# Performance work log

Measured on AMD Instinct MI355X. Metric: run time of the kernel, lower is better.

Reference implementation:

```python
import jax, jax.numpy as jnp
import numpy as np

N_NODES = 131072
IN_F = 512
HID = 512
H = 8
DH = HID // H
B = 1024  # batch_size (num graphs); static for jit
LN_EPS = 1e-5


def setup_inputs() -> dict:
    key = jax.random.key(0)
    ks = jax.random.split(key, 12)
    # equal-size segments (128 nodes/graph), sorted as in PyG batching
    batch = (jnp.arange(N_NODES) // (N_NODES // B)).astype(jnp.int32)
    s = 0.02
    return {
        "x": jax.random.normal(ks[0], (N_NODES, IN_F), jnp.float32),
        "batch": batch,
        "query": jax.random.normal(ks[1], (H, DH), jnp.float32) * s,
        "key_w": jax.random.normal(ks[2], (HID, IN_F), jnp.float32) * s,
        "key_b": jnp.zeros((HID,), jnp.float32),
        "value_w": jax.random.normal(ks[3], (HID, IN_F), jnp.float32) * s,
        "value_b": jnp.zeros((HID,), jnp.float32),
        "out_w": jax.random.normal(ks[4], (IN_F, HID), jnp.float32) * s,
        "out_b": jnp.zeros((IN_F,), jnp.float32),
        "gate_w": jax.random.normal(ks[5], (IN_F, 2 * IN_F), jnp.float32) * s,
        "gate_b": jnp.zeros((IN_F,), jnp.float32),
        "ln_w": jnp.ones((IN_F,), jnp.float32),
        "ln_b": jnp.zeros((IN_F,), jnp.float32),
    }


def reference(x, batch, query, key_w, key_b, value_w, value_b, out_w, out_b,
              gate_w, gate_b, ln_w, ln_b):
    N = x.shape[0]
    # projections (dense GEMMs)
    keys = (x @ key_w.T + key_b).reshape(N, H, DH)
    values = (x @ value_w.T + value_b).reshape(N, H, DH)
    # per-node attention logits against shared per-head query: [N, H]
    scores = jnp.einsum('nhd,hd->nh', keys, query)
    # segment softmax over nodes within each graph
    smax = jax.ops.segment_max(scores, batch, num_segments=B)  # [B, H]
    smax = jnp.where(jnp.isfinite(smax), smax, 0.0)            # guard empty graphs
    e = jnp.exp(scores - smax[batch])
    ssum = jax.ops.segment_sum(e, batch, num_segments=B)       # [B, H]
    w = e / jnp.maximum(ssum[batch], 1e-12)                    # [N, H]  (dropout is eval-mode identity)
    # attention-weighted pooling of values: [B, H, DH] -> [B, HID]
    pooled = jax.ops.segment_sum(w[:, :, None] * values, batch, num_segments=B)
    ctx = pooled.reshape(B, HID) @ out_w.T + out_b             # [B, IN_F]
    # gating with per-graph mean pool
    counts = jax.ops.segment_sum(jnp.ones((N,), x.dtype), batch, num_segments=B)
    avg = jax.ops.segment_sum(x, batch, num_segments=B) / jnp.maximum(counts, 1.0)[:, None]
    gate = jax.nn.sigmoid(jnp.concatenate([ctx, avg], axis=1) @ gate_w.T + gate_b)
    ctx = gate * ctx + (1.0 - gate) * avg
    emb = jnp.where(counts[:, None] > 0, ctx, 0.0)             # empty graphs stay zero
    # LayerNorm
    mu = emb.mean(-1, keepdims=True)
    var = emb.var(-1, keepdims=True)
    return (emb - mu) / jnp.sqrt(var + LN_EPS) * ln_w + ln_b
```

## Files before the change

### kernel.cpp

```cpp
#include <hip/hip_runtime.h>
#include <hip/hip_bf16.h>

typedef short short8 __attribute__((ext_vector_type(8)));
typedef float f32x4 __attribute__((ext_vector_type(4)));

#define NGRAPH 1024
#define NPG    128
#define INF    512
#define NHEAD  8
#define CH     32

__device__ __forceinline__ ushort f2b(float f){
  __hip_bfloat16 h(f);
  union { __hip_bfloat16 h; ushort u; } v; v.h = h; return v.u;
}
__device__ __forceinline__ float b2f_lo(unsigned u){
  union { unsigned u; float f; } v; v.u = u << 16; return v.f;
}
__device__ __forceinline__ float b2f_hi(unsigned u){
  union { unsigned u; float f; } v; v.u = u & 0xffff0000u; return v.f;
}

__global__ void k_prep(const float* __restrict__ q, const float* __restrict__ kw,
                       float* __restrict__ kq,
                       const float* __restrict__ vw, ushort* __restrict__ vwb,
                       const float* __restrict__ ow, ushort* __restrict__ owb,
                       const float* __restrict__ gw, ushort* __restrict__ gwb){
  const int b = blockIdx.x, t = threadIdx.x;
  if(b < 16){
    int h = b >> 1, f = (b & 1)*256 + t;
    float s = 0.f;
    #pragma unroll 8
    for(int d = 0; d < 64; d++)
      s += q[h*64 + d] * kw[(size_t)(h*64 + d)*INF + f];
    kq[h*INF + f] = s;
  } else if(b < 16 + 1024){
    int i = (b - 16)*256 + t;   vwb[i] = f2b(vw[i]);
  } else if(b < 16 + 2048){
    int i = (b - 1040)*256 + t; owb[i] = f2b(ow[i]);
  } else {
    int i = (b - 2064)*256 + t; gwb[i] = f2b(gw[i]);
  }
}

__global__ __launch_bounds__(128, 2) void k_graph(
    const float* __restrict__ x, const float* __restrict__ kq,
    ushort* __restrict__ xw_b, float* __restrict__ avg_f, ushort* __restrict__ avg_b){
  __shared__ __align__(16) ushort xs[CH*INF];
  __shared__ __align__(16) float  sc[CH*NHEAD];
  __shared__ float mEf[3*NHEAD];

  const int t = threadIdx.x, lane = t & 63, w = t >> 6;
  const int col = lane & 15, kg = lane >> 4;
  const int g = blockIdx.x;
  const int node = w*16 + col;

  short8 bfrag[16];
  {
    const bool ok = (col < 8);
    const float* kqr = kq + col*INF;
    #pragma unroll
    for(int ks = 0; ks < 16; ks++){
      short8 v = short8{0,0,0,0,0,0,0,0};
      if(ok){
        float4 p0 = *(const float4*)(kqr + ks*32 + kg*8);
        float4 p1 = *(const float4*)(kqr + ks*32 + kg*8 + 4);
        v[0]=(short)f2b(p0.x); v[1]=(short)f2b(p0.y); v[2]=(short)f2b(p0.z); v[3]=(short)f2b(p0.w);
        v[4]=(short)f2b(p1.x); v[5]=(short)f2b(p1.y); v[6]=(short)f2b(p1.z); v[7]=(short)f2b(p1.w);
      }
      bfrag[ks] = v;
    }
  }

  if(t < NHEAD){ mEf[t] = -1e30f; mEf[NHEAD + t] = 0.f; }

  float acc[NHEAD][4];
  #pragma unroll
  for(int h = 0; h < NHEAD; h++)
    #pragma unroll
    for(int j = 0; j < 4; j++) acc[h][j] = 0.f;
  float cs[4] = {0.f, 0.f, 0.f, 0.f};

  for(int c = 0; c < 4; c++){
    {
      const float* xr = x + (size_t)(g*NPG + c*CH + node)*INF + kg*8;
      f32x4 sacc = {0.f,0.f,0.f,0.f};
      #pragma unroll
      for(int ks = 0; ks < 16; ks++){
        float4 a = *(const float4*)(xr + ks*32);
        float4 b = *(const float4*)(xr + ks*32 + 4);
        short8 af;
        af[0]=(short)f2b(a.x); af[1]=(short)f2b(a.y); af[2]=(short)f2b(a.z); af[3]=(short)f2b(a.w);
        af[4]=(short)f2b(b.x); af[5]=(short)f2b(b.y); af[6]=(short)f2b(b.z); af[7]=(short)f2b(b.w);
        *(short8*)((char*)xs + node*1024 + ((ks*64 + kg*16) ^ ((node & 7) << 4))) = af;
        sacc = __builtin_amdgcn_mfma_f32_16x16x32_bf16(af, bfrag[ks], sacc, 0, 0, 0);
      }
      if(col < 8){
        #pragma unroll
        for(int r = 0; r < 4; r++)
          sc[(w*16 + kg*4 + r)*NHEAD + col] = sacc[r];
      }
    }
    __syncthreads();

    {
      int h = t >> 4, s = t & 15;
      float v[2]; float m = -1e30f;
      #pragma unroll
      for(int i = 0; i < 2; i++){ v[i] = sc[(s + 16*i)*NHEAD + h]; m = fmaxf(m, v[i]); }
      #pragma unroll
      for(int msk = 1; msk < 16; msk <<= 1) m = fmaxf(m, __shfl_xor(m, msk));
      float es = 0.f;
      #pragma unroll
      for(int i = 0; i < 2; i++){ v[i] = __expf(v[i] - m); es += v[i]; }
      #pragma unroll
      for(int msk = 1; msk < 16; msk <<= 1) es += __shfl_xor(es, msk);
      float M = mEf[h], E = mEf[NHEAD + h];
      float Mn = fmaxf(M, m);
      float f_old = __expf(M - Mn), f_new = __expf(m - Mn);
      #pragma unroll
      for(int i = 0; i < 2; i++) sc[(s + 16*i)*NHEAD + h] = v[i]*f_new;
      if(s == 0){
        mEf[h] = Mn;
        mEf[NHEAD + h] = E*f_old + es*f_new;
        mEf[2*NHEAD + h] = f_old;
      }
    }
    __syncthreads();

    {
      float fo[NHEAD];
      #pragma unroll
      for(int h = 0; h < NHEAD; h++) fo[h] = mEf[2*NHEAD + h];
      #pragma unroll
      for(int h = 0; h < NHEAD; h++)
        #pragma unroll
        for(int j = 0; j < 4; j++) acc[h][j] *= fo[h];
      #pragma unroll 4
      for(int n = 0; n < CH; n++){
        uint2 xv = *(const uint2*)((const char*)xs + n*1024 + ((8*t) ^ ((n & 7) << 4)));
        float x0 = b2f_lo(xv.x), x1 = b2f_hi(xv.x);
        float x2 = b2f_lo(xv.y), x3 = b2f_hi(xv.y);
        float4 w0 = *(float4*)(sc + n*NHEAD);
        float4 w1 = *(float4*)(sc + n*NHEAD + 4);
        float wv[8] = {w0.x, w0.y, w0.z, w0.w, w1.x, w1.y, w1.z, w1.w};
        #pragma unroll
        for(int h = 0; h < NHEAD; h++){
          acc[h][0] += wv[h]*x0; acc[h][1] += wv[h]*x1;
          acc[h][2] += wv[h]*x2; acc[h][3] += wv[h]*x3;
        }
        cs[0] += x0; cs[1] += x1; cs[2] += x2; cs[3] += x3;
      }
    }
    __syncthreads();
  }

  #pragma unroll
  for(int h = 0; h < NHEAD; h++){
    float einv = 1.0f / fmaxf(mEf[NHEAD + h], 1e-12f);
    float v0 = acc[h][0]*einv, v1 = acc[h][1]*einv;
    float v2 = acc[h][2]*einv, v3 = acc[h][3]*einv;
    uint2 pk = { (unsigned)f2b(v0) | ((unsigned)f2b(v1) << 16),
                 (unsigned)f2b(v2) | ((unsigned)f2b(v3) << 16) };
    *(uint2*)(xw_b + (size_t)g*4096 + h*INF + 4*t) = pk;
  }
  float am0 = cs[0]*(1.0f/128.0f), am1 = cs[1]*(1.0f/128.0f);
  float am2 = cs[2]*(1.0f/128.0f), am3 = cs[3]*(1.0f/128.0f);
  float4 av = {am0, am1, am2, am3};
  *(float4*)(avg_f + (size_t)g*INF + 4*t) = av;
  uint2 pk = { (unsigned)f2b(am0) | ((unsigned)f2b(am1) << 16),
               (unsigned)f2b(am2) | ((unsigned)f2b(am3) << 16) };
  *(uint2*)(avg_b + (size_t)g*INF + 4*t) = pk;
}

__global__ __launch_bounds__(256, 2) void gemm_tn(
    const ushort* __restrict__ A1, const ushort* __restrict__ A2,
    int lda, int headmode,
    const ushort* __restrict__ Wt, int ldw,
    const float* __restrict__ bias,
    float* __restrict__ Cf, ushort* __restrict__ Cb,
    int ldc, int K, int ksplit){
  __shared__ ushort As[2][64*72];
  __shared__ ushort Bs[2][64*72];
  const int t = threadIdx.x, lane = t & 63, w = t >> 6;
  const int m0 = blockIdx.x*64, n0 = blockIdx.y*64;
  const int aoff = headmode ? blockIdx.y*512 : 0;
  const int col = lane & 15, kg = lane >> 4;
  const int lr = t >> 2, lk = (t & 3)*16;

  f32x4 acc[2][2];
  #pragma unroll
  for(int i = 0; i < 2; i++)
    #pragma unroll
    for(int j = 0; j < 2; j++) acc[i][j] = f32x4{0.f,0.f,0.f,0.f};

  const ushort* Ap0 = (0 < ksplit) ? A1 : A2;
  short8 va0 = *(const short8*)(Ap0 + (size_t)(m0 + lr)*lda + aoff + lk);
  short8 va1 = *(const short8*)(Ap0 + (size_t)(m0 + lr)*lda + aoff + lk + 8);
  short8 vb0 = *(const short8*)(Wt + (size_t)(n0 + lr)*ldw + lk);
  short8 vb1 = *(const short8*)(Wt + (size_t)(n0 + lr)*ldw + lk + 8);
  int buf = 0;
  for(int kc = 0; kc < K; kc += 64){
    *(short8*)((char*)&As[buf][0] + lr*144 + lk*2)      = va0;
    *(short8*)((char*)&As[buf][0] + lr*144 + lk*2 + 16) = va1;
    *(short8*)((char*)&Bs[buf][0] + lr*144 + lk*2)      = vb0;
    *(short8*)((char*)&Bs[buf][0] + lr*144 + lk*2 + 16) = vb1;
    __syncthreads();
    if(kc + 64 < K){
      int kn = kc + 64;
      const ushort* Ap = (kn < ksplit) ? A1 : A2;
      int kl = (kn < ksplit) ? kn : kn - ksplit;
      va0 = *(const short8*)(Ap + (size_t)(m0 + lr)*lda + aoff + kl + lk);
      va1 = *(const short8*)(Ap + (size_t)(m0 + lr)*lda + aoff + kl + lk + 8);
      vb0 = *(const short8*)(Wt + (size_t)(n0 + lr)*ldw + kn + lk);
      vb1 = *(const short8*)(Wt + (size_t)(n0 + lr)*ldw + kn + lk + 8);
    }
    const int mr = (w & 1)*32, nc = (w >> 1)*32;
    #pragma unroll
    for(int kk = 0; kk < 2; kk++){
      short8 af0 = *(short8*)((char*)&As[buf][0] + (mr + col)*144      + kk*64 + kg*16);
      short8 af1 = *(short8*)((char*)&As[buf][0] + (mr + 16 + col)*144 + kk*64 + kg*16);
      short8 bf0 = *(short8*)((char*)&Bs[buf][0] + (nc + col)*144      + kk*64 + kg*16);
      short8 bf1 = *(short8*)((char*)&Bs[buf][0] + (nc + 16 + col)*144 + kk*64 + kg*16);
      acc[0][0] = __builtin_amdgcn_mfma_f32_16x16x32_bf16(af0, bf0, acc[0][0], 0,0,0);
      acc[0][1] = __builtin_amdgcn_mfma_f32_16x16x32_bf16(af0, bf1, acc[0][1], 0,0,0);
      acc[1][0] = __builtin_amdgcn_mfma_f32_16x16x32_bf16(af1, bf0, acc[1][0], 0,0,0);
      acc[1][1] = __builtin_amdgcn_mfma_f32_16x16x32_bf16(af1, bf1, acc[1][1], 0,0,0);
    }
    buf ^= 1;
  }
  #pragma unroll
  for(int mi = 0; mi < 2; mi++)
    #pragma unroll
    for(int ni = 0; ni < 2; ni++)
      #pragma unroll
      for(int r = 0; r < 4; r++){
        int rr = m0 + (w & 1)*32 + mi*16 + kg*4 + r;
        int cc = n0 + (w >> 1)*32 + ni*16 + col;
        float vv = acc[mi][ni][r] + bias[cc];
        if(Cf) Cf[(size_t)rr*ldc + cc] = vv;
        if(Cb) Cb[(size_t)rr*ldc + cc] = f2b(vv);
      }
}

__global__ __launch_bounds__(512, 2) void k5_epilogue(
    const float* __restrict__ z, const float* __restrict__ ctx,
    const float* __restrict__ avg, const float* __restrict__ lnw,
    const float* __restrict__ lnb, float* __restrict__ out){
  __shared__ float red[16];
  const int t = threadIdx.x, b = blockIdx.x;
  const size_t i = (size_t)b*INF + t;
  float zz = z[i], c = ctx[i], a = avg[i];
  float g = 1.0f / (1.0f + __expf(-zz));
  float e = g*c + (1.0f - g)*a;
  float s1 = e, s2 = e*e;
  #pragma unroll
  for(int m = 1; m < 64; m <<= 1){ s1 += __shfl_xor(s1, m); s2 += __shfl_xor(s2, m); }
  int wv = t >> 6;
  if((t & 63) == 0){ red[wv] = s1; red[8 + wv] = s2; }
  __syncthreads();
  float ts1 = 0.f, ts2 = 0.f;
  #pragma unroll
  for(int k = 0; k < 8; k++){ ts1 += red[k]; ts2 += red[8 + k]; }
  float mu = ts1 * (1.0f/512.0f);
  float var = ts2 * (1.0f/512.0f) - mu*mu;
  out[i] = (e - mu) * rsqrtf(var + 1e-5f) * lnw[t] + lnb[t];
}

extern "C" void kernel_launch(void* const* d_in, const int* in_sizes, int n_in,
                              void* d_out, int out_size, void* d_ws, size_t ws_size,
                              hipStream_t stream){
  const float* x       = (const float*)d_in[0];
  const float* query   = (const float*)d_in[2];
  const float* key_w   = (const float*)d_in[3];
  const float* value_w = (const float*)d_in[5];
  const float* value_b = (const float*)d_in[6];
  const float* out_w   = (const float*)d_in[7];
  const float* out_b   = (const float*)d_in[8];
  const float* gate_w  = (const float*)d_in[9];
  const float* gate_b  = (const float*)d_in[10];
  const float* ln_w    = (const float*)d_in[11];
  const float* ln_b    = (const float*)d_in[12];
  float* out = (float*)d_out;

  char* ws = (char*)d_ws;
  float*  kq       = (float*) (ws + 0);
  ushort* vw_b     = (ushort*)(ws + 16384);
  ushort* ow_b     = (ushort*)(ws + 540672);
  ushort* gw_b     = (ushort*)(ws + 1064960);
  ushort* xw_b     = (ushort*)(ws + 2113536);
  float*  avg_f    = (float*) (ws + 10502144);
  ushort* avg_b    = (ushort*)(ws + 12599296);
  ushort* pooled_b = (ushort*)(ws + 13647872);
  float*  ctx_f    = (float*) (ws + 14696448);
  ushort* ctx_b    = (ushort*)(ws + 16793600);
  float*  z_f      = (float*) (ws + 17842176);

  k_prep<<<4112, 256, 0, stream>>>(query, key_w, kq, value_w, vw_b,
                                   out_w, ow_b, gate_w, gw_b);

  k_graph<<<NGRAPH, 128, 0, stream>>>(x, kq, xw_b, avg_f, avg_b);

  gemm_tn<<<dim3(16, 8), 256, 0, stream>>>(xw_b, xw_b, 4096, 1, vw_b, 512, value_b,
                                           nullptr, pooled_b, 512, 512, 1 << 30);
  gemm_tn<<<dim3(16, 8), 256, 0, stream>>>(pooled_b, pooled_b, 512, 0, ow_b, 512, out_b,
                                           ctx_f, ctx_b, 512, 512, 1 << 30);
  gemm_tn<<<dim3(16, 8), 256, 0, stream>>>(ctx_b, avg_b, 512, 0, gw_b, 1024, gate_b,
                                           z_f, nullptr, 512, 1024, 512);

  k5_epilogue<<<NGRAPH, 512, 0, stream>>>(z_f, ctx_f, avg_f, ln_w, ln_b, out);
}
```

Measured before the change: 97.34 us.

## Double the k_graph block to 256 threads and prefetch the next x chunk into registers

The graph kernel now runs 256 threads per block. Each thread prefetches its part of the next 32-node chunk of x into registers while the current chunk is pooled. The fp32 rows are converted to bf16 and stored cooperatively into shared memory, and the kq fragment is staged in LDS instead of being held in per-thread registers. Only two waves run the MFMA score computation from LDS, and the pooling work per thread is halved to two columns. The aim is to hide global load latency and raise occupancy, at the cost of extra LDS traffic, a further barrier per chunk, and idle waves during the score phase.

```diff
diff --git a/kernel.cpp b/kernel.cpp
--- a/kernel.cpp
+++ b/kernel.cpp
@@ -43,57 +43,68 @@
   }
 }
 
-__global__ __launch_bounds__(128, 2) void k_graph(
+__global__ __launch_bounds__(256, 3) void k_graph(
     const float* __restrict__ x, const float* __restrict__ kq,
     ushort* __restrict__ xw_b, float* __restrict__ avg_f, ushort* __restrict__ avg_b){
   __shared__ __align__(16) ushort xs[CH*INF];
+  __shared__ __align__(16) ushort kqs[16*64*8];
   __shared__ __align__(16) float  sc[CH*NHEAD];
   __shared__ float mEf[3*NHEAD];
 
   const int t = threadIdx.x, lane = t & 63, w = t >> 6;
-  const int col = lane & 15, kg = lane >> 4;
+  const int w8 = w*8;
   const int g = blockIdx.x;
-  const int node = w*16 + col;
-
-  short8 bfrag[16];
+
+  float4 pf[16];
   {
-    const bool ok = (col < 8);
-    const float* kqr = kq + col*INF;
-    #pragma unroll
-    for(int ks = 0; ks < 16; ks++){
-      short8 v = short8{0,0,0,0,0,0,0,0};
-      if(ok){
-        float4 p0 = *(const float4*)(kqr + ks*32 + kg*8);
-        float4 p1 = *(const float4*)(kqr + ks*32 + kg*8 + 4);
-        v[0]=(short)f2b(p0.x); v[1]=(short)f2b(p0.y); v[2]=(short)f2b(p0.z); v[3]=(short)f2b(p0.w);
-        v[4]=(short)f2b(p1.x); v[5]=(short)f2b(p1.y); v[6]=(short)f2b(p1.z); v[7]=(short)f2b(p1.w);
-      }
-      bfrag[ks] = v;
-    }
-  }
-
+    const float* xc = x + (size_t)(g*NPG + w8)*INF;
+    #pragma unroll
+    for(int s = 0; s < 16; s++)
+      pf[s] = *(const float4*)(xc + (s>>1)*INF + (s&1)*256 + lane*4);
+  }
+
+  #pragma unroll
+  for(int i = 0; i < 4; i++){
+    int idx = t*4 + i;
+    int ks = idx >> 6, ln = idx & 63;
+    int cc = ln & 15, kg2 = ln >> 4;
+    short8 v = short8{0,0,0,0,0,0,0,0};
+    if(cc < 8){
+      const float* kqr = kq + cc*INF + ks*32 + kg2*8;
+      float4 p0 = *(const float4*)(kqr);
+      float4 p1 = *(const float4*)(kqr + 4);
+      v[0]=(short)f2b(p0.x); v[1]=(short)f2b(p0.y); v[2]=(short)f2b(p0.z); v[3]=(short)f2b(p0.w);
+      v[4]=(short)f2b(p1.x); v[5]=(short)f2b(p1.y); v[6]=(short)f2b(p1.z); v[7]=(short)f2b(p1.w);
+    }
+    *(short8*)((char*)kqs + (ks*64 + ln)*16) = v;
+  }
   if(t < NHEAD){ mEf[t] = -1e30f; mEf[NHEAD + t] = 0.f; }
 
-  float acc[NHEAD][4];
-  #pragma unroll
-  for(int h = 0; h < NHEAD; h++)
-    #pragma unroll
-    for(int j = 0; j < 4; j++) acc[h][j] = 0.f;
-  float cs[4] = {0.f, 0.f, 0.f, 0.f};
+  float acc[NHEAD][2];
+  #pragma unroll
+  for(int h = 0; h < NHEAD; h++){ acc[h][0] = 0.f; acc[h][1] = 0.f; }
+  float cs0 = 0.f, cs1 = 0.f;
 
   for(int c = 0; c < 4; c++){
-    {
-      const float* xr = x + (size_t)(g*NPG + c*CH + node)*INF + kg*8;
+    #pragma unroll
+    for(int s = 0; s < 16; s++){
+      int nd = w8 + (s>>1);
+      int cb = (s&1)*512 + lane*8;
+      ushort4 v;
+      v.x = f2b(pf[s].x); v.y = f2b(pf[s].y); v.z = f2b(pf[s].z); v.w = f2b(pf[s].w);
+      *(ushort4*)((char*)xs + nd*1024 + (cb ^ ((nd & 7) << 4))) = v;
+    }
+    __syncthreads();
+
+    if(w < 2){
+      const int col = lane & 15, kg = lane >> 4;
+      const int node = w*16 + col;
       f32x4 sacc = {0.f,0.f,0.f,0.f};
       #pragma unroll
       for(int ks = 0; ks < 16; ks++){
-        float4 a = *(const float4*)(xr + ks*32);
-        float4 b = *(const float4*)(xr + ks*32 + 4);
-        short8 af;
-        af[0]=(short)f2b(a.x); af[1]=(short)f2b(a.y); af[2]=(short)f2b(a.z); af[3]=(short)f2b(a.w);
-        af[4]=(short)f2b(b.x); af[5]=(short)f2b(b.y); af[6]=(short)f2b(b.z); af[7]=(short)f2b(b.w);
-        *(short8*)((char*)xs + node*1024 + ((ks*64 + kg*16) ^ ((node & 7) << 4))) = af;
-        sacc = __builtin_amdgcn_mfma_f32_16x16x32_bf16(af, bfrag[ks], sacc, 0, 0, 0);
+        short8 af = *(short8*)((char*)xs + node*1024 + ((ks*64 + kg*16) ^ ((node & 7) << 4)));
+        short8 bf = *(short8*)((char*)kqs + (ks*64 + lane)*16);
+        sacc = __builtin_amdgcn_mfma_f32_16x16x32_bf16(af, bf, sacc, 0, 0, 0);
       }
       if(col < 8){
         #pragma unroll
@@ -103,7 +114,7 @@
     }
     __syncthreads();
 
-    {
+    if(t < 128){
       int h = t >> 4, s = t & 15;
       float v[2]; float m = -1e30f;
       #pragma unroll
@@ -129,27 +140,29 @@
     __syncthreads();
 
     {
-      float fo[NHEAD];
-      #pragma unroll
-      for(int h = 0; h < NHEAD; h++) fo[h] = mEf[2*NHEAD + h];
-      #pragma unroll
-      for(int h = 0; h < NHEAD; h++)
+      #pragma unroll
+      for(int h = 0; h < NHEAD; h++){
+        float fo = mEf[2*NHEAD + h];
+        acc[h][0] *= fo; acc[h][1] *= fo;
+      }
+      if(c < 3){
+        const float* xn = x + (size_t)(g*NPG + (c+1)*CH + w8)*INF;
         #pragma unroll
-        for(int j = 0; j < 4; j++) acc[h][j] *= fo[h];
+        for(int s = 0; s < 16; s++)
+          pf[s] = *(const float4*)(xn + (s>>1)*INF + (s&1)*256 + lane*4);
+      }
       #pragma unroll 4
       for(int n = 0; n < CH; n++){
-        uint2 xv = *(const uint2*)((const char*)xs + n*1024 + ((8*t) ^ ((n & 7) << 4)));
-        float x0 = b2f_lo(xv.x), x1 = b2f_hi(xv.x);
-        float x2 = b2f_lo(xv.y), x3 = b2f_hi(xv.y);
+        unsigned xv = *(const unsigned*)((const char*)xs + n*1024 + ((4*t) ^ ((n & 7) << 4)));
+        float x0 = b2f_lo(xv), x1 = b2f_hi(xv);
         float4 w0 = *(float4*)(sc + n*NHEAD);
         float4 w1 = *(float4*)(sc + n*NHEAD + 4);
         float wv[8] = {w0.x, w0.y, w0.z, w0.w, w1.x, w1.y, w1.z, w1.w};
         #pragma unroll
         for(int h = 0; h < NHEAD; h++){
           acc[h][0] += wv[h]*x0; acc[h][1] += wv[h]*x1;
-          acc[h][2] += wv[h]*x2; acc[h][3] += wv[h]*x3;
         }
-        cs[0] += x0; cs[1] += x1; cs[2] += x2; cs[3] += x3;
+        cs0 += x0; cs1 += x1;
       }
     }
     __syncthreads();
@@ -159,18 +172,14 @@
   for(int h = 0; h < NHEAD; h++){
     float einv = 1.0f / fmaxf(mEf[NHEAD + h], 1e-12f);
     float v0 = acc[h][0]*einv, v1 = acc[h][1]*einv;
-    float v2 = acc[h][2]*einv, v3 = acc[h][3]*einv;
-    uint2 pk = { (unsigned)f2b(v0) | ((unsigned)f2b(v1) << 16),
-                 (unsigned)f2b(v2) | ((unsigned)f2b(v3) << 16) };
-    *(uint2*)(xw_b + (size_t)g*4096 + h*INF + 4*t) = pk;
-  }
-  float am0 = cs[0]*(1.0f/128.0f), am1 = cs[1]*(1.0f/128.0f);
-  float am2 = cs[2]*(1.0f/128.0f), am3 = cs[3]*(1.0f/128.0f);
-  float4 av = {am0, am1, am2, am3};
-  *(float4*)(avg_f + (size_t)g*INF + 4*t) = av;
-  uint2 pk = { (unsigned)f2b(am0) | ((unsigned)f2b(am1) << 16),
-               (unsigned)f2b(am2) | ((unsigned)f2b(am3) << 16) };
-  *(uint2*)(avg_b + (size_t)g*INF + 4*t) = pk;
+    unsigned pk = (unsigned)f2b(v0) | ((unsigned)f2b(v1) << 16);
+    *(unsigned*)(xw_b + (size_t)g*4096 + h*INF + 2*t) = pk;
+  }
+  float am0 = cs0*(1.0f/128.0f), am1 = cs1*(1.0f/128.0f);
+  float2 av = {am0, am1};
+  *(float2*)(avg_f + (size_t)g*INF + 2*t) = av;
+  unsigned pk = (unsigned)f2b(am0) | ((unsigned)f2b(am1) << 16);
+  *(unsigned*)(avg_b + (size_t)g*INF + 2*t) = pk;
 }
 
 __global__ __launch_bounds__(256, 2) void gemm_tn(
@@ -299,7 +308,7 @@
   k_prep<<<4112, 256, 0, stream>>>(query, key_w, kq, value_w, vw_b,
                                    out_w, ow_b, gate_w, gw_b);
 
-  k_graph<<<NGRAPH, 128, 0, stream>>>(x, kq, xw_b, avg_f, avg_b);
+  k_graph<<<NGRAPH, 256, 0, stream>>>(x, kq, xw_b, avg_f, avg_b);
 
   gemm_tn<<<dim3(16, 8), 256, 0, stream>>>(xw_b, xw_b, 4096, 1, vw_b, 512, value_b,
                                            nullptr, pooled_b, 512, 512, 1 << 30);
```

After: 98.17 us. Within noise of the previous version (+0.9%).

## Fold weight bf16 conversion into GEMM loads and halve GEMM M-tile

Applied to the files above, without the earlier changes.

Removes the separate prep pass that converted value, out and gate weights to bf16. The GEMMs now load fp32 weights directly and convert them to bf16 while staging into shared memory. The GEMM M tile is halved to 32 rows so the grid has twice as many blocks, and the occupancy hint is raised to 4. The cost is more weight traffic, because each block reads fp32 weights and more blocks re-read the same weight tiles, plus extra conversion instructions inside the GEMM loop.

```diff
diff --git a/kernel.cpp b/kernel.cpp
--- a/kernel.cpp
+++ b/kernel.cpp
@@ -21,26 +21,14 @@
   union { unsigned u; float f; } v; v.u = u & 0xffff0000u; return v.f;
 }
 
-__global__ void k_prep(const float* __restrict__ q, const float* __restrict__ kw,
-                       float* __restrict__ kq,
-                       const float* __restrict__ vw, ushort* __restrict__ vwb,
-                       const float* __restrict__ ow, ushort* __restrict__ owb,
-                       const float* __restrict__ gw, ushort* __restrict__ gwb){
-  const int b = blockIdx.x, t = threadIdx.x;
-  if(b < 16){
-    int h = b >> 1, f = (b & 1)*256 + t;
-    float s = 0.f;
-    #pragma unroll 8
-    for(int d = 0; d < 64; d++)
-      s += q[h*64 + d] * kw[(size_t)(h*64 + d)*INF + f];
-    kq[h*INF + f] = s;
-  } else if(b < 16 + 1024){
-    int i = (b - 16)*256 + t;   vwb[i] = f2b(vw[i]);
-  } else if(b < 16 + 2048){
-    int i = (b - 1040)*256 + t; owb[i] = f2b(ow[i]);
-  } else {
-    int i = (b - 2064)*256 + t; gwb[i] = f2b(gw[i]);
-  }
+__global__ void k_kq(const float* __restrict__ q, const float* __restrict__ kw,
+                     float* __restrict__ kq){
+  int h = blockIdx.x, t = threadIdx.x;
+  float s = 0.f;
+  #pragma unroll 8
+  for(int d = 0; d < 64; d++)
+    s += q[h*64 + d] * kw[(size_t)(h*64 + d)*INF + t];
+  kq[h*INF + t] = s;
 }
 
 __global__ __launch_bounds__(128, 2) void k_graph(
@@ -173,74 +161,76 @@
   *(uint2*)(avg_b + (size_t)g*INF + 4*t) = pk;
 }
 
-__global__ __launch_bounds__(256, 2) void gemm_tn(
+__global__ __launch_bounds__(256, 4) void gemm_tn(
     const ushort* __restrict__ A1, const ushort* __restrict__ A2,
     int lda, int headmode,
-    const ushort* __restrict__ Wt, int ldw,
+    const float* __restrict__ Wt, int ldw,
     const float* __restrict__ bias,
     float* __restrict__ Cf, ushort* __restrict__ Cb,
     int ldc, int K, int ksplit){
-  __shared__ ushort As[2][64*72];
+  __shared__ ushort As[2][32*72];
   __shared__ ushort Bs[2][64*72];
   const int t = threadIdx.x, lane = t & 63, w = t >> 6;
-  const int m0 = blockIdx.x*64, n0 = blockIdx.y*64;
+  const int m0 = blockIdx.x*32, n0 = blockIdx.y*64;
   const int aoff = headmode ? blockIdx.y*512 : 0;
   const int col = lane & 15, kg = lane >> 4;
-  const int lr = t >> 2, lk = (t & 3)*16;
-
-  f32x4 acc[2][2];
-  #pragma unroll
-  for(int i = 0; i < 2; i++)
-    #pragma unroll
-    for(int j = 0; j < 2; j++) acc[i][j] = f32x4{0.f,0.f,0.f,0.f};
+  const int ar = t >> 3, ak = (t & 7)*8;
+  const int br = t >> 2, bk = (t & 3)*16;
+
+  f32x4 acc[2];
+  acc[0] = f32x4{0.f,0.f,0.f,0.f};
+  acc[1] = f32x4{0.f,0.f,0.f,0.f};
 
   const ushort* Ap0 = (0 < ksplit) ? A1 : A2;
-  short8 va0 = *(const short8*)(Ap0 + (size_t)(m0 + lr)*lda + aoff + lk);
-  short8 va1 = *(const short8*)(Ap0 + (size_t)(m0 + lr)*lda + aoff + lk + 8);
-  short8 vb0 = *(const short8*)(Wt + (size_t)(n0 + lr)*ldw + lk);
-  short8 vb1 = *(const short8*)(Wt + (size_t)(n0 + lr)*ldw + lk + 8);
+  short8 va = *(const short8*)(Ap0 + (size_t)(m0 + ar)*lda + aoff + ak);
+  float4 wb0 = *(const float4*)(Wt + (size_t)(n0 + br)*ldw + bk);
+  float4 wb1 = *(const float4*)(Wt + (size_t)(n0 + br)*ldw + bk + 4);
+  float4 wb2 = *(const float4*)(Wt + (size_t)(n0 + br)*ldw + bk + 8);
+  float4 wb3 = *(const float4*)(Wt + (size_t)(n0 + br)*ldw + bk + 12);
   int buf = 0;
   for(int kc = 0; kc < K; kc += 64){
-    *(short8*)((char*)&As[buf][0] + lr*144 + lk*2)      = va0;
-    *(short8*)((char*)&As[buf][0] + lr*144 + lk*2 + 16) = va1;
-    *(short8*)((char*)&Bs[buf][0] + lr*144 + lk*2)      = vb0;
-    *(short8*)((char*)&Bs[buf][0] + lr*144 + lk*2 + 16) = vb1;
+    *(short8*)((char*)&As[buf][0] + ar*144 + ak*2) = va;
+    {
+      short8 b0, b1;
+      b0[0]=(short)f2b(wb0.x); b0[1]=(short)f2b(wb0.y); b0[2]=(short)f2b(wb0.z); b0[3]=(short)f2b(wb0.w);
+      b0[4]=(short)f2b(wb1.x); b0[5]=(short)f2b(wb1.y); b0[6]=(short)f2b(wb1.z); b0[7]=(short)f2b(wb1.w);
+      b1[0]=(short)f2b(wb2.x); b1[1]=(short)f2b(wb2.y); b1[2]=(short)f2b(wb2.z); b1[3]=(short)f2b(wb2.w);
+      b1[4]=(short)f2b(wb3.x); b1[5]=(short)f2b(wb3.y); b1[6]=(short)f2b(wb3.z); b1[7]=(short)f2b(wb3.w);
+      *(short8*)((char*)&Bs[buf][0] + br*144 + bk*2)      = b0;
+      *(short8*)((char*)&Bs[buf][0] + br*144 + bk*2 + 16) = b1;
+    }
     __syncthreads();
     if(kc + 64 < K){
       int kn = kc + 64;
       const ushort* Ap = (kn < ksplit) ? A1 : A2;
       int kl = (kn < ksplit) ? kn : kn - ksplit;
-      va0 = *(const short8*)(Ap + (size_t)(m0 + lr)*lda + aoff + kl + lk);
-      va1 = *(const short8*)(Ap + (size_t)(m0 + lr)*lda + aoff + kl + lk + 8);
-      vb0 = *(const short8*)(Wt + (size_t)(n0 + lr)*ldw + kn + lk);
-      vb1 = *(const short8*)(Wt + (size_t)(n0 + lr)*ldw + kn + lk + 8);
-    }
-    const int mr = (w & 1)*32, nc = (w >> 1)*32;
+      va  = *(const short8*)(Ap + (size_t)(m0 + ar)*lda + aoff + kl + ak);
+      wb0 = *(const float4*)(Wt + (size_t)(n0 + br)*ldw + kn + bk);
+      wb1 = *(const float4*)(Wt + (size_t)(n0 + br)*ldw + kn + bk + 4);
+      wb2 = *(const float4*)(Wt + (size_t)(n0 + br)*ldw + kn + bk + 8);
+      wb3 = *(const float4*)(Wt + (size_t)(n0 + br)*ldw + kn + bk + 12);
+    }
+    const int mr = (w & 1)*16, nc = (w >> 1)*32;
     #pragma unroll
     for(int kk = 0; kk < 2; kk++){
-      short8 af0 = *(short8*)((char*)&As[buf][0] + (mr + col)*144      + kk*64 + kg*16);
-      short8 af1 = *(short8*)((char*)&As[buf][0] + (mr + 16 + col)*144 + kk*64 + kg*16);
+      short8 af  = *(short8*)((char*)&As[buf][0] + (mr + col)*144      + kk*64 + kg*16);
       short8 bf0 = *(short8*)((char*)&Bs[buf][0] + (nc + col)*144      + kk*64 + kg*16);
       short8 bf1 = *(short8*)((char*)&Bs[buf][0] + (nc + 16 + col)*144 + kk*64 + kg*16);
-      acc[0][0] = __builtin_amdgcn_mfma_f32_16x16x32_bf16(af0, bf0, acc[0][0], 0,0,0);
-      acc[0][1] = __builtin_amdgcn_mfma_f32_16x16x32_bf16(af0, bf1, acc[0][1], 0,0,0);
-      acc[1][0] = __builtin_amdgcn_mfma_f32_16x16x32_bf16(af1, bf0, acc[1][0], 0,0,0);
-      acc[1][1] = __builtin_amdgcn_mfma_f32_16x16x32_bf16(af1, bf1, acc[1][1], 0,0,0);
+      acc[0] = __builtin_amdgcn_mfma_f32_16x16x32_bf16(af, bf0, acc[0], 0,0,0);
+      acc[1] = __builtin_amdgcn_mfma_f32_16x16x32_bf16(af, bf1, acc[1], 0,0,0);
     }
     buf ^= 1;
   }
   #pragma unroll
-  for(int mi = 0; mi < 2; mi++)
-    #pragma unroll
-    for(int ni = 0; ni < 2; ni++)
-      #pragma unroll
-      for(int r = 0; r < 4; r++){
-        int rr = m0 + (w & 1)*32 + mi*16 + kg*4 + r;
-        int cc = n0 + (w >> 1)*32 + ni*16 + col;
-        float vv = acc[mi][ni][r] + bias[cc];
-        if(Cf) Cf[(size_t)rr*ldc + cc] = vv;
-        if(Cb) Cb[(size_t)rr*ldc + cc] = f2b(vv);
-      }
+  for(int ni = 0; ni < 2; ni++)
+    #pragma unroll
+    for(int r = 0; r < 4; r++){
+      int rr = m0 + (w & 1)*16 + kg*4 + r;
+      int cc = n0 + (w >> 1)*32 + ni*16 + col;
+      float vv = acc[ni][r] + bias[cc];
+      if(Cf) Cf[(size_t)rr*ldc + cc] = vv;
+      if(Cb) Cb[(size_t)rr*ldc + cc] = f2b(vv);
+    }
 }
 
 __global__ __launch_bounds__(512, 2) void k5_epilogue(
@@ -285,27 +275,23 @@
 
   char* ws = (char*)d_ws;
   float*  kq       = (float*) (ws + 0);
-  ushort* vw_b     = (ushort*)(ws + 16384);
-  ushort* ow_b     = (ushort*)(ws + 540672);
-  ushort* gw_b     = (ushort*)(ws + 1064960);
-  ushort* xw_b     = (ushort*)(ws + 2113536);
-  float*  avg_f    = (float*) (ws + 10502144);
-  ushort* avg_b    = (ushort*)(ws + 12599296);
-  ushort* pooled_b = (ushort*)(ws + 13647872);
-  float*  ctx_f    = (float*) (ws + 14696448);
-  ushort* ctx_b    = (ushort*)(ws + 16793600);
-  float*  z_f      = (float*) (ws + 17842176);
-
-  k_prep<<<4112, 256, 0, stream>>>(query, key_w, kq, value_w, vw_b,
-                                   out_w, ow_b, gate_w, gw_b);
+  ushort* xw_b     = (ushort*)(ws + 16384);
+  float*  avg_f    = (float*) (ws + 8404992);
+  ushort* avg_b    = (ushort*)(ws + 10502144);
+  ushort* pooled_b = (ushort*)(ws + 11550720);
+  float*  ctx_f    = (float*) (ws + 12599296);
+  ushort* ctx_b    = (ushort*)(ws + 14696448);
+  float*  z_f      = (float*) (ws + 15745024);
+
+  k_kq<<<8, 512, 0, stream>>>(query, key_w, kq);
 
   k_graph<<<NGRAPH, 128, 0, stream>>>(x, kq, xw_b, avg_f, avg_b);
 
-  gemm_tn<<<dim3(16, 8), 256, 0, stream>>>(xw_b, xw_b, 4096, 1, vw_b, 512, value_b,
+  gemm_tn<<<dim3(32, 8), 256, 0, stream>>>(xw_b, xw_b, 4096, 1, value_w, 512, value_b,
                                            nullptr, pooled_b, 512, 512, 1 << 30);
-  gemm_tn<<<dim3(16, 8), 256, 0, stream>>>(pooled_b, pooled_b, 512, 0, ow_b, 512, out_b,
+  gemm_tn<<<dim3(32, 8), 256, 0, stream>>>(pooled_b, pooled_b, 512, 0, out_w, 512, out_b,
                                            ctx_f, ctx_b, 512, 512, 1 << 30);
-  gemm_tn<<<dim3(16, 8), 256, 0, stream>>>(ctx_b, avg_b, 512, 0, gw_b, 1024, gate_b,
+  gemm_tn<<<dim3(32, 8), 256, 0, stream>>>(ctx_b, avg_b, 512, 0, gate_w, 1024, gate_b,
                                            z_f, nullptr, 512, 1024, 512);
 
   k5_epilogue<<<NGRAPH, 512, 0, stream>>>(z_f, ctx_f, avg_f, ln_w, ln_b, out);
```

Measured after the change: 99.42 us. 2.1% more time.

## Fuse value, output, gate GEMMs and LayerNorm epilogue into one kernel

Applied to the files above, without the earlier changes.

Replaces three tiled GEMM launches and the epilogue kernel with a single kernel in which each block handles 16 graphs end to end. Pooled, context and gate intermediates are kept in swizzled shared memory instead of being written to and reread from global memory. The cost is only 64 blocks, which uses a small share of the GPU. Each block also streams the full weight matrices directly from global or L2 without LDS reuse.

```diff
diff --git a/kernel.cpp b/kernel.cpp
--- a/kernel.cpp
+++ b/kernel.cpp
@@ -173,98 +173,125 @@
   *(uint2*)(avg_b + (size_t)g*INF + 4*t) = pk;
 }
 
-__global__ __launch_bounds__(256, 2) void gemm_tn(
-    const ushort* __restrict__ A1, const ushort* __restrict__ A2,
-    int lda, int headmode,
-    const ushort* __restrict__ Wt, int ldw,
-    const float* __restrict__ bias,
-    float* __restrict__ Cf, ushort* __restrict__ Cb,
-    int ldc, int K, int ksplit){
-  __shared__ ushort As[2][64*72];
-  __shared__ ushort Bs[2][64*72];
+__global__ __launch_bounds__(256, 1) void k_tail(
+    const ushort* __restrict__ xw, const ushort* __restrict__ vwb,
+    const float* __restrict__ vb,  const ushort* __restrict__ owb,
+    const float* __restrict__ ob,  const ushort* __restrict__ gwb,
+    const float* __restrict__ gb,  const ushort* __restrict__ avgb,
+    const float* __restrict__ avgf, const float* __restrict__ lnw,
+    const float* __restrict__ lnb, float* __restrict__ out){
+  __shared__ __align__(16) ushort pooled[16*512];
+  __shared__ __align__(16) float  ctxf[16*512];
+  __shared__ __align__(16) ushort ctxb[16*512];
+  __shared__ __align__(16) float  zf[16*512];
+
   const int t = threadIdx.x, lane = t & 63, w = t >> 6;
-  const int m0 = blockIdx.x*64, n0 = blockIdx.y*64;
-  const int aoff = headmode ? blockIdx.y*512 : 0;
   const int col = lane & 15, kg = lane >> 4;
-  const int lr = t >> 2, lk = (t & 3)*16;
-
-  f32x4 acc[2][2];
+  const int r0 = blockIdx.x*16;
+
   #pragma unroll
-  for(int i = 0; i < 2; i++)
-    #pragma unroll
-    for(int j = 0; j < 2; j++) acc[i][j] = f32x4{0.f,0.f,0.f,0.f};
-
-  const ushort* Ap0 = (0 < ksplit) ? A1 : A2;
-  short8 va0 = *(const short8*)(Ap0 + (size_t)(m0 + lr)*lda + aoff + lk);
-  short8 va1 = *(const short8*)(Ap0 + (size_t)(m0 + lr)*lda + aoff + lk + 8);
-  short8 vb0 = *(const short8*)(Wt + (size_t)(n0 + lr)*ldw + lk);
-  short8 vb1 = *(const short8*)(Wt + (size_t)(n0 + lr)*ldw + lk + 8);
-  int buf = 0;
-  for(int kc = 0; kc < K; kc += 64){
-    *(short8*)((char*)&As[buf][0] + lr*144 + lk*2)      = va0;
-    *(short8*)((char*)&As[buf][0] + lr*144 + lk*2 + 16) = va1;
-    *(short8*)((char*)&Bs[buf][0] + lr*144 + lk*2)      = vb0;
-    *(short8*)((char*)&Bs[buf][0] + lr*144 + lk*2 + 16) = vb1;
+  for(int hh = 0; hh < 2; hh++){
+    const int h = w*2 + hh;
+    f32x4 acc[4];
+    #pragma unroll
+    for(int nt = 0; nt < 4; nt++) acc[nt] = f32x4{0.f,0.f,0.f,0.f};
+    for(int ks = 0; ks < 16; ks++){
+      short8 af = *(const short8*)(xw + (size_t)(r0 + col)*4096 + h*512 + ks*32 + kg*8);
+      #pragma unroll
+      for(int nt = 0; nt < 4; nt++){
+        short8 bf = *(const short8*)(vwb + (size_t)(h*64 + nt*16 + col)*512 + ks*32 + kg*8);
+        acc[nt] = __builtin_amdgcn_mfma_f32_16x16x32_bf16(af, bf, acc[nt], 0,0,0);
+      }
+    }
+    #pragma unroll
+    for(int nt = 0; nt < 4; nt++)
+      #pragma unroll
+      for(int r = 0; r < 4; r++){
+        int row = kg*4 + r, cc = h*64 + nt*16 + col;
+        float v = acc[nt][r] + vb[cc];
+        *(ushort*)((char*)pooled + row*1024 + ((cc*2) ^ ((row & 7) << 4))) = f2b(v);
+      }
+  }
+  __syncthreads();
+
+  {
+    f32x4 acc[8];
+    #pragma unroll
+    for(int ni = 0; ni < 8; ni++) acc[ni] = f32x4{0.f,0.f,0.f,0.f};
+    for(int ks = 0; ks < 16; ks++){
+      short8 af = *(short8*)((char*)pooled + col*1024 + (((ks*32 + kg*8)*2) ^ ((col & 7) << 4)));
+      #pragma unroll
+      for(int ni = 0; ni < 8; ni++){
+        short8 bf = *(const short8*)(owb + (size_t)((w*8 + ni)*16 + col)*512 + ks*32 + kg*8);
+        acc[ni] = __builtin_amdgcn_mfma_f32_16x16x32_bf16(af, bf, acc[ni], 0,0,0);
+      }
+    }
     __syncthreads();
-    if(kc + 64 < K){
-      int kn = kc + 64;
-      const ushort* Ap = (kn < ksplit) ? A1 : A2;
-      int kl = (kn < ksplit) ? kn : kn - ksplit;
-      va0 = *(const short8*)(Ap + (size_t)(m0 + lr)*lda + aoff + kl + lk);
-      va1 = *(const short8*)(Ap + (size_t)(m0 + lr)*lda + aoff + kl + lk + 8);
-      vb0 = *(const short8*)(Wt + (size_t)(n0 + lr)*ldw + kn + lk);
-      vb1 = *(const short8*)(Wt + (size_t)(n0 + lr)*ldw + kn + lk + 8);
-    }
-    const int mr = (w & 1)*32, nc = (w >> 1)*32;
-    #pragma unroll
-    for(int kk = 0; kk < 2; kk++){
-      short8 af0 = *(short8*)((char*)&As[buf][0] + (mr + col)*144      + kk*64 + kg*16);
-      short8 af1 = *(short8*)((char*)&As[buf][0] + (mr + 16 + col)*144 + kk*64 + kg*16);
-      short8 bf0 = *(short8*)((char*)&Bs[buf][0] + (nc + col)*144      + kk*64 + kg*16);
-      short8 bf1 = *(short8*)((char*)&Bs[buf][0] + (nc + 16 + col)*144 + kk*64 + kg*16);
-      acc[0][0] = __builtin_amdgcn_mfma_f32_16x16x32_bf16(af0, bf0, acc[0][0], 0,0,0);
-      acc[0][1] = __builtin_amdgcn_mfma_f32_16x16x32_bf16(af0, bf1, acc[0][1], 0,0,0);
-      acc[1][0] = __builtin_amdgcn_mfma_f32_16x16x32_bf16(af1, bf0, acc[1][0], 0,0,0);
-      acc[1][1] = __builtin_amdgcn_mfma_f32_16x16x32_bf16(af1, bf1, acc[1][1], 0,0,0);
-    }
-    buf ^= 1;
-  }
-  #pragma unroll
-  for(int mi = 0; mi < 2; mi++)
-    #pragma unroll
-    for(int ni = 0; ni < 2; ni++)
+    #pragma unroll
+    for(int ni = 0; ni < 8; ni++)
       #pragma unroll
       for(int r = 0; r < 4; r++){
-        int rr = m0 + (w & 1)*32 + mi*16 + kg*4 + r;
-        int cc = n0 + (w >> 1)*32 + ni*16 + col;
-        float vv = acc[mi][ni][r] + bias[cc];
-        if(Cf) Cf[(size_t)rr*ldc + cc] = vv;
-        if(Cb) Cb[(size_t)rr*ldc + cc] = f2b(vv);
-      }
-}
-
-__global__ __launch_bounds__(512, 2) void k5_epilogue(
-    const float* __restrict__ z, const float* __restrict__ ctx,
-    const float* __restrict__ avg, const float* __restrict__ lnw,
-    const float* __restrict__ lnb, float* __restrict__ out){
-  __shared__ float red[16];
-  const int t = threadIdx.x, b = blockIdx.x;
-  const size_t i = (size_t)b*INF + t;
-  float zz = z[i], c = ctx[i], a = avg[i];
-  float g = 1.0f / (1.0f + __expf(-zz));
-  float e = g*c + (1.0f - g)*a;
-  float s1 = e, s2 = e*e;
-  #pragma unroll
-  for(int m = 1; m < 64; m <<= 1){ s1 += __shfl_xor(s1, m); s2 += __shfl_xor(s2, m); }
-  int wv = t >> 6;
-  if((t & 63) == 0){ red[wv] = s1; red[8 + wv] = s2; }
+        int row = kg*4 + r, cc = (w*8 + ni)*16 + col;
+        float v = acc[ni][r] + ob[cc];
+        ctxf[row*512 + cc] = v;
+        *(ushort*)((char*)ctxb + row*1024 + ((cc*2) ^ ((row & 7) << 4))) = f2b(v);
+      }
+  }
   __syncthreads();
-  float ts1 = 0.f, ts2 = 0.f;
-  #pragma unroll
-  for(int k = 0; k < 8; k++){ ts1 += red[k]; ts2 += red[8 + k]; }
-  float mu = ts1 * (1.0f/512.0f);
-  float var = ts2 * (1.0f/512.0f) - mu*mu;
-  out[i] = (e - mu) * rsqrtf(var + 1e-5f) * lnw[t] + lnb[t];
+
+  {
+    f32x4 zacc[8];
+    #pragma unroll
+    for(int ni = 0; ni < 8; ni++) zacc[ni] = f32x4{0.f,0.f,0.f,0.f};
+    for(int ks = 0; ks < 32; ks++){
+      short8 af;
+      if(ks < 16)
+        af = *(short8*)((char*)ctxb + col*1024 + (((ks*32 + kg*8)*2) ^ ((col & 7) << 4)));
+      else
+        af = *(const short8*)(avgb + (size_t)(r0 + col)*512 + (ks - 16)*32 + kg*8);
+      #pragma unroll
+      for(int ni = 0; ni < 8; ni++){
+        short8 bf = *(const short8*)(gwb + (size_t)((w*8 + ni)*16 + col)*1024 + ks*32 + kg*8);
+        zacc[ni] = __builtin_amdgcn_mfma_f32_16x16x32_bf16(af, bf, zacc[ni], 0,0,0);
+      }
+    }
+    #pragma unroll
+    for(int ni = 0; ni < 8; ni++)
+      #pragma unroll
+      for(int r = 0; r < 4; r++){
+        int row = kg*4 + r, cc = (w*8 + ni)*16 + col;
+        zf[row*512 + cc] = zacc[ni][r] + gb[cc];
+      }
+  }
+  __syncthreads();
+
+  {
+    const int row = t >> 4, j = t & 15;
+    float e[32];
+    float s1 = 0.f, s2 = 0.f;
+    #pragma unroll
+    for(int i = 0; i < 32; i++){
+      int cc = j + i*16;
+      float zz = zf[row*512 + cc];
+      float cv = ctxf[row*512 + cc];
+      float av = avgf[(size_t)(r0 + row)*512 + cc];
+      float gg = 1.0f / (1.0f + __expf(-zz));
+      float ee = gg*cv + (1.0f - gg)*av;
+      e[i] = ee; s1 += ee; s2 += ee*ee;
+    }
+    #pragma unroll
+    for(int msk = 1; msk < 16; msk <<= 1){
+      s1 += __shfl_xor(s1, msk); s2 += __shfl_xor(s2, msk);
+    }
+    float mu = s1*(1.0f/512.0f);
+    float var = s2*(1.0f/512.0f) - mu*mu;
+    float rinv = rsqrtf(var + 1e-5f);
+    #pragma unroll
+    for(int i = 0; i < 32; i++){
+      int cc = j + i*16;
+      out[(size_t)(r0 + row)*512 + cc] = (e[i] - mu)*rinv*lnw[cc] + lnb[cc];
+    }
+  }
 }
 
 extern "C" void kernel_launch(void* const* d_in, const int* in_sizes, int n_in,
@@ -284,29 +311,19 @@
   float* out = (float*)d_out;
 
   char* ws = (char*)d_ws;
-  float*  kq       = (float*) (ws + 0);
-  ushort* vw_b     = (ushort*)(ws + 16384);
-  ushort* ow_b     = (ushort*)(ws + 540672);
-  ushort* gw_b     = (ushort*)(ws + 1064960);
-  ushort* xw_b     = (ushort*)(ws + 2113536);
-  float*  avg_f    = (float*) (ws + 10502144);
-  ushort* avg_b    = (ushort*)(ws + 12599296);
-  ushort* pooled_b = (ushort*)(ws + 13647872);
-  float*  ctx_f    = (float*) (ws + 14696448);
-  ushort* ctx_b    = (ushort*)(ws + 16793600);
-  float*  z_f      = (float*) (ws + 17842176);
+  float*  kq    = (float*) (ws + 0);
+  ushort* vw_b  = (ushort*)(ws + 16384);
+  ushort* ow_b  = (ushort*)(ws + 540672);
+  ushort* gw_b  = (ushort*)(ws + 1064960);
+  ushort* xw_b  = (ushort*)(ws + 2113536);
+  float*  avg_f = (float*) (ws + 10502144);
+  ushort* avg_b = (ushort*)(ws + 12599296);
 
   k_prep<<<4112, 256, 0, stream>>>(query, key_w, kq, value_w, vw_b,
                                    out_w, ow_b, gate_w, gw_b);
 
   k_graph<<<NGRAPH, 128, 0, stream>>>(x, kq, xw_b, avg_f, avg_b);
 
-  gemm_tn<<<dim3(16, 8), 256, 0, stream>>>(xw_b, xw_b, 4096, 1, vw_b, 512, value_b,
-                                           nullptr, pooled_b, 512, 512, 1 << 30);
-  gemm_tn<<<dim3(16, 8), 256, 0, stream>>>(pooled_b, pooled_b, 512, 0, ow_b, 512, out_b,
-                                           ctx_f, ctx_b, 512, 512, 1 << 30);
-  gemm_tn<<<dim3(16, 8), 256, 0, stream>>>(ctx_b, avg_b, 512, 0, gw_b, 1024, gate_b,
-                                           z_f, nullptr, 512, 1024, 512);
-
-  k5_epilogue<<<NGRAPH, 512, 0, stream>>>(z_f, ctx_f, avg_f, ln_w, ln_b, out);
-}
+  k_tail<<<64, 256, 0, stream>>>(xw_b, vw_b, value_b, ow_b, out_b, gw_b, gate_b,
+                                 avg_b, avg_f, ln_w, ln_b, out);
+}
```

Result: slower. 135.4 us (+39.1%).
